# Kernel tuning notes

Hardware: AMD Instinct MI355X
Metric: run time of the kernel (lower is better)

The kernel has to match this reference:

```python
import jax, jax.numpy as jnp
import numpy as np

B, C, M, K, V, D, H, A, L, HF = 2, 128, 4, 4, 64, 1024, 16, 64, 4, 2048
E = M + K
EPS = 1e-5
THETA = 10000.0


def _rmsnorm(x, w):
    return x * jax.lax.rsqrt(jnp.mean(x * x, -1, keepdims=True) + EPS) * w


def _l2norm(x):
    n = jnp.sqrt(jnp.sum(x * x, -1, keepdims=True))
    return x / jnp.maximum(n, EPS)


def _rope(x, cos, sin):
    x1, x2 = jnp.split(x, 2, axis=-1)
    return jnp.concatenate([x1 * cos + x2 * sin, -x1 * sin + x2 * cos], -1)


def _forward(x_input, dec_w1, dec_w2, pos_emb, Wqkv, Wo, Wup, Wdown, attn_norm_w, ffn_norm_w, doc):
    b = x_input.shape[0]
    c = x_input.shape[1] // M
    # decoder_w1 then 'b (c m) (k v) -> b c k (m v)', decoder_w2, pos emb
    x = jnp.einsum('bsd,od->bso', x_input, dec_w1)
    x = x.reshape(b, c, M, K, V).transpose(0, 1, 3, 2, 4).reshape(b, c, K, M * V)
    x = jnp.einsum('bcku,du->bckd', x, dec_w2) + pos_emb
    # decoder_include_original_token: prepend original m tokens per block
    x = jnp.concatenate([x_input.reshape(b, c, M, D), x], axis=2).reshape(b, c * E, D)
    s = c * E
    # mask_mod (decoder_global_original_attn): (causal & kv%e<k & same_doc) | same_block
    idx = jnp.arange(s)
    blk = idx // E
    docs = doc[:, blk]  # [b, s]
    doc_m = docs[:, :, None] == docs[:, None, :]
    causal = blk[:, None] >= blk[None, :]
    kv_ok = (idx % E) < K
    same = blk[:, None] == blk[None, :]
    mask = (causal[None] & kv_ok[None, None, :] & doc_m) | same[None]  # [b, s, s]
    # rotary tables (applied post head-split, dim A)
    inv_freq = (1.0 / THETA) ** (jnp.arange(0, A, 2) / A)
    freqs = jnp.arange(s)[:, None] * inv_freq[None, :]
    cos, sin = jnp.cos(freqs), jnp.sin(freqs)  # [s, A/2]
    scale = 1.0 / jnp.sqrt(jnp.float32(A))
    neg = jnp.float32(-1e30)

    def heads(t):
        return t.reshape(b, s, H, A).transpose(0, 2, 1, 3)

    for li in range(L):
        xn = _rmsnorm(x, attn_norm_w[li])
        qkv = jnp.einsum('bsd,od->bso', xn, Wqkv[li])
        q, k, v = jnp.split(qkv, 3, axis=-1)
        q, k, v = heads(q), heads(k), heads(v)
        q, k = _l2norm(q), _l2norm(k)  # qk_norm
        q, k = _rope(q, cos, sin), _rope(k, cos, sin)
        scores = jnp.einsum('bhqa,bhka->bhqk', q, k) * scale
        scores = jnp.where(mask[:, None], scores, neg)
        probs = jax.nn.softmax(scores, axis=-1)
        attn = jnp.einsum('bhqk,bhka->bhqa', probs, v)
        attn = attn.transpose(0, 2, 1, 3).reshape(b, s, D)
        x1_in = jnp.einsum('bsd,od->bso', attn, Wo[li]) + x
        xf = _rmsnorm(x1_in, ffn_norm_w[li])
        up = jnp.einsum('bsd,od->bso', xf, Wup[li])
        u1, u2 = jnp.split(up, 2, axis=-1)
        x = jnp.einsum('bsh,dh->bsd', jax.nn.silu(u1) * u2, Wdown[li]) + x1_in
    # 'b (c e) d -> (b c) e d' then drop original tokens
    return x.reshape(b * c, E, D)[:, M:]


def setup_inputs() -> dict:
    key = jax.random.key(0)
    ks = jax.random.split(key, 10)
    sc = 0.02
    return {
        'x_input': jax.random.normal(ks[0], (B, C * M, D), jnp.float32),
        'doc': jnp.sort(jax.random.randint(ks[1], (B, C), 0, 4), axis=-1),
        'dec_w1': jax.random.normal(ks[2], (K * V, D), jnp.float32) * sc,
        'dec_w2': jax.random.normal(ks[3], (D, M * V), jnp.float32) * sc,
        'pos_emb': jax.random.normal(ks[4], (1, 1, K, D), jnp.float32) * sc,
        'Wqkv': jax.random.normal(ks[5], (L, 3 * D, D), jnp.float32) * sc,
        'Wo': jax.random.normal(ks[6], (L, D, D), jnp.float32) * sc,
        'Wup': jax.random.normal(ks[7], (L, 2 * HF, D), jnp.float32) * sc,
        'Wdown': jax.random.normal(ks[8], (L, D, HF), jnp.float32) * sc,
        'attn_norm_w': jnp.ones((L, D), jnp.float32),
        'ffn_norm_w': jnp.ones((L, D), jnp.float32),
    }


def reference(x_input, doc, dec_w1, dec_w2, pos_emb, Wqkv, Wo, Wup, Wdown, attn_norm_w, ffn_norm_w):
    return _forward(x_input, dec_w1, dec_w2, pos_emb, Wqkv, Wo, Wup, Wdown, attn_norm_w, ffn_norm_w, doc)
```

## Files before the change

kernel.cpp:

```cpp
#include <hip/hip_runtime.h>
#include <hip/hip_bf16.h>

typedef __bf16 bf16;
typedef __bf16 bf16x8 __attribute__((ext_vector_type(8)));
typedef __bf16 bf16x4 __attribute__((ext_vector_type(4)));
typedef float  f32x4  __attribute__((ext_vector_type(4)));

#define MFMA16(a, b, c) __builtin_amdgcn_mfma_f32_16x16x32_bf16(a, b, c, 0, 0, 0)

template <int EPI, int AF32, int BF32, int TM, int TN>
__global__ __launch_bounds__(256) void gemm_bt(
    const void* __restrict__ Av, const void* __restrict__ Bv,
    const float* __restrict__ Res, void* __restrict__ Out,
    int Ntot, int Ktot, int lda)
{
    constexpr int PA = TM / 64, PB = TN / 64;
    constexpr int WN = (TN == 128) ? ((TM == 128) ? 2 : 4) : 2;
    constexpr int WM = 4 / WN;
    constexpr int I = TM / (WM * 16), J = TN / (WN * 16);
    __shared__ __align__(16) bf16 As[2][TM][40];
    __shared__ __align__(16) bf16 Bs[2][TN][40];
    const int tid  = threadIdx.x;
    const int wave = tid >> 6, lane = tid & 63;
    const int quad = lane >> 4, l16 = lane & 15;
    const int wm = wave / WN, wn = wave % WN;
    const int rowW = wm * (TM / WM), colW = wn * (TN / WN);
    const int rowBase = blockIdx.y * TM, colBase = blockIdx.x * TN;

    f32x4 acc[I][J];
    const f32x4 z4 = {0.f, 0.f, 0.f, 0.f};
#pragma unroll
    for (int i = 0; i < I; i++)
#pragma unroll
        for (int j = 0; j < J; j++) acc[i][j] = z4;

    float4 rAf[PA][2]; bf16x8 rAb[PA];
    float4 rBf[PB][2]; bf16x8 rBb[PB];

    auto loadTile = [&](int kt) {
#pragma unroll
        for (int p = 0; p < PA; p++) {
            int ch = p * 256 + tid, r = ch >> 2, c8 = (ch & 3) << 3;
            if (AF32) {
                const float* s = (const float*)Av + (size_t)(rowBase + r) * lda + kt + c8;
                rAf[p][0] = *(const float4*)s; rAf[p][1] = *(const float4*)(s + 4);
            } else {
                rAb[p] = *(const bf16x8*)((const bf16*)Av + (size_t)(rowBase + r) * lda + kt + c8);
            }
        }
#pragma unroll
        for (int p = 0; p < PB; p++) {
            int ch = p * 256 + tid, r = ch >> 2, c8 = (ch & 3) << 3;
            if (BF32) {
                const float* s = (const float*)Bv + (size_t)(colBase + r) * Ktot + kt + c8;
                rBf[p][0] = *(const float4*)s; rBf[p][1] = *(const float4*)(s + 4);
            } else {
                rBb[p] = *(const bf16x8*)((const bf16*)Bv + (size_t)(colBase + r) * Ktot + kt + c8);
            }
        }
    };
    auto storeTile = [&](int buf) {
#pragma unroll
        for (int p = 0; p < PA; p++) {
            int ch = p * 256 + tid, r = ch >> 2, c8 = (ch & 3) << 3;
            bf16x8 t;
            if (AF32) {
                t[0]=(bf16)rAf[p][0].x; t[1]=(bf16)rAf[p][0].y; t[2]=(bf16)rAf[p][0].z; t[3]=(bf16)rAf[p][0].w;
                t[4]=(bf16)rAf[p][1].x; t[5]=(bf16)rAf[p][1].y; t[6]=(bf16)rAf[p][1].z; t[7]=(bf16)rAf[p][1].w;
            } else t = rAb[p];
            *(bf16x8*)&As[buf][r][c8] = t;
        }
#pragma unroll
        for (int p = 0; p < PB; p++) {
            int ch = p * 256 + tid, r = ch >> 2, c8 = (ch & 3) << 3;
            bf16x8 t;
            if (BF32) {
                t[0]=(bf16)rBf[p][0].x; t[1]=(bf16)rBf[p][0].y; t[2]=(bf16)rBf[p][0].z; t[3]=(bf16)rBf[p][0].w;
                t[4]=(bf16)rBf[p][1].x; t[5]=(bf16)rBf[p][1].y; t[6]=(bf16)rBf[p][1].z; t[7]=(bf16)rBf[p][1].w;
            } else t = rBb[p];
            *(bf16x8*)&Bs[buf][r][c8] = t;
        }
    };

    loadTile(0);
    storeTile(0);
    __syncthreads();
    const int nk = Ktot >> 5;
    for (int k = 0; k < nk; k++) {
        const bool more = (k + 1) < nk;
        if (more) loadTile((k + 1) << 5);
        const int buf = k & 1;
        bf16x8 af[I], bfr[J];
#pragma unroll
        for (int i = 0; i < I; i++)
            af[i] = *(const bf16x8*)&As[buf][rowW + i * 16 + l16][quad * 8];
#pragma unroll
        for (int j = 0; j < J; j++)
            bfr[j] = *(const bf16x8*)&Bs[buf][colW + j * 16 + l16][quad * 8];
#pragma unroll
        for (int i = 0; i < I; i++)
#pragma unroll
            for (int j = 0; j < J; j++)
                acc[i][j] = MFMA16(af[i], bfr[j], acc[i][j]);
        if (more) { storeTile(buf ^ 1); __syncthreads(); }
    }

#pragma unroll
    for (int i = 0; i < I; i++) {
        int row0 = rowBase + rowW + i * 16 + quad * 4;
#pragma unroll
        for (int j = 0; j < J; j++) {
            int col = colBase + colW + j * 16 + l16;
#pragma unroll
            for (int r = 0; r < 4; r++) {
                size_t off = (size_t)(row0 + r) * Ntot + col;
                float v = acc[i][j][r];
                if (EPI == 0)      ((bf16*)Out)[off]  = (bf16)v;
                else if (EPI == 1) ((float*)Out)[off] = v + Res[off];
                else               ((float*)Out)[off] = v;
            }
        }
    }
}

__global__ __launch_bounds__(256) void gemm_up_swiglu(
    const bf16* __restrict__ A, const float* __restrict__ B,
    bf16* __restrict__ Out)
{
    __shared__ __align__(16) bf16 As[2][128][40];
    __shared__ __align__(16) bf16 Bs[2][128][40];
    const int tid  = threadIdx.x;
    const int wave = tid >> 6, lane = tid & 63;
    const int quad = lane >> 4, l16 = lane & 15;
    const int wm = wave >> 1, wn = wave & 1;
    const int rowBase = blockIdx.y * 128, cb = blockIdx.x;

    f32x4 acc[4][4];
    const f32x4 z4 = {0.f, 0.f, 0.f, 0.f};
#pragma unroll
    for (int i = 0; i < 4; i++)
#pragma unroll
        for (int j = 0; j < 4; j++) acc[i][j] = z4;

    bf16x8 rA[2]; float4 rB[2][2];
    auto loadTile = [&](int kt) {
#pragma unroll
        for (int p = 0; p < 2; p++) {
            int ch = p * 256 + tid, r = ch >> 2, c8 = (ch & 3) << 3;
            rA[p] = *(const bf16x8*)(A + (size_t)(rowBase + r) * 1024 + kt + c8);
            int brow = (r >> 6) * 2048 + cb * 64 + (r & 63);
            const float* s = B + (size_t)brow * 1024 + kt + c8;
            rB[p][0] = *(const float4*)s; rB[p][1] = *(const float4*)(s + 4);
        }
    };
    auto storeTile = [&](int buf) {
#pragma unroll
        for (int p = 0; p < 2; p++) {
            int ch = p * 256 + tid, r = ch >> 2, c8 = (ch & 3) << 3;
            *(bf16x8*)&As[buf][r][c8] = rA[p];
            bf16x8 t;
            t[0]=(bf16)rB[p][0].x; t[1]=(bf16)rB[p][0].y; t[2]=(bf16)rB[p][0].z; t[3]=(bf16)rB[p][0].w;
            t[4]=(bf16)rB[p][1].x; t[5]=(bf16)rB[p][1].y; t[6]=(bf16)rB[p][1].z; t[7]=(bf16)rB[p][1].w;
            *(bf16x8*)&Bs[buf][r][c8] = t;
        }
    };

    loadTile(0);
    storeTile(0);
    __syncthreads();
    for (int k = 0; k < 32; k++) {
        const bool more = k < 31;
        if (more) loadTile((k + 1) << 5);
        const int buf = k & 1;
        bf16x8 af[4], bfr[4];
#pragma unroll
        for (int i = 0; i < 4; i++)
            af[i] = *(const bf16x8*)&As[buf][wm * 64 + i * 16 + l16][quad * 8];
#pragma unroll
        for (int j = 0; j < 4; j++) {
            int brow = (j < 2) ? (wn * 32 + j * 16) : (64 + wn * 32 + (j - 2) * 16);
            bfr[j] = *(const bf16x8*)&Bs[buf][brow + l16][quad * 8];
        }
#pragma unroll
        for (int i = 0; i < 4; i++)
#pragma unroll
            for (int j = 0; j < 4; j++)
                acc[i][j] = MFMA16(af[i], bfr[j], acc[i][j]);
        if (more) { storeTile(buf ^ 1); __syncthreads(); }
    }

#pragma unroll
    for (int i = 0; i < 4; i++) {
        int row0 = rowBase + wm * 64 + i * 16 + quad * 4;
#pragma unroll
        for (int jj = 0; jj < 2; jj++) {
            int col = cb * 64 + wn * 32 + jj * 16 + l16;
#pragma unroll
            for (int r = 0; r < 4; r++) {
                float u1 = acc[i][jj][r], u2 = acc[i][jj + 2][r];
                float g = u1 / (1.f + __expf(-u1));
                Out[(size_t)(row0 + r) * 2048 + col] = (bf16)(g * u2);
            }
        }
    }
}

__global__ __launch_bounds__(256) void rmsnorm_k(
    const float* __restrict__ X, const float* __restrict__ W,
    bf16* __restrict__ Out)
{
    const int row = blockIdx.x, tid = threadIdx.x;
    const float4 xv = *(const float4*)(X + (size_t)row * 1024 + tid * 4);
    float ss = xv.x * xv.x + xv.y * xv.y + xv.z * xv.z + xv.w * xv.w;
#pragma unroll
    for (int m = 1; m < 64; m <<= 1) ss += __shfl_xor(ss, m);
    __shared__ float red[4];
    if ((tid & 63) == 0) red[tid >> 6] = ss;
    __syncthreads();
    float tot = red[0] + red[1] + red[2] + red[3];
    float sc = rsqrtf(tot * (1.0f / 1024.0f) + 1e-5f);
    const float4 wv = *(const float4*)(W + tid * 4);
    bf16x4 o;
    o[0] = (bf16)(xv.x * sc * wv.x);
    o[1] = (bf16)(xv.y * sc * wv.y);
    o[2] = (bf16)(xv.z * sc * wv.z);
    o[3] = (bf16)(xv.w * sc * wv.w);
    *(bf16x4*)(Out + (size_t)row * 1024 + tid * 4) = o;
}

__global__ __launch_bounds__(256) void ropetab_k(float* __restrict__ tab)
{
    int i = blockIdx.x * 256 + threadIdx.x;
    int s = i >> 5, j = i & 31;
    float f = (float)s * __expf(-(float)j * 0.2878231366242557f);
    tab[i * 2]     = cosf(f);
    tab[i * 2 + 1] = sinf(f);
}

__global__ __launch_bounds__(256) void qkprep_k(
    bf16* __restrict__ qkv, const float* __restrict__ tab)
{
    int wid  = blockIdx.x * 4 + (threadIdx.x >> 6);
    int lane = threadIdx.x & 63;
    int s = wid & 1023, h = (wid >> 10) & 15, b = (wid >> 14) & 1, op = wid >> 15;
    bf16* addr = qkv + ((size_t)(b * 1024 + s)) * 3072 + op * 1024 + h * 64 + lane;
    float v = (float)*addr;
    float ss = v * v;
#pragma unroll
    for (int m = 1; m < 64; m <<= 1) ss += __shfl_xor(ss, m);
    v /= fmaxf(sqrtf(ss), 1e-5f);
    float2 cssn = ((const float2*)tab)[(s << 5) + (lane & 31)];
    float partner = __shfl_xor(v, 32);
    float o = (lane < 32) ? (v * cssn.x + partner * cssn.y)
                          : (v * cssn.x - partner * cssn.y);
    if (op == 0) o *= 0.125f;
    *addr = (bf16)o;
}

__global__ __launch_bounds__(256) void vtrans_k(
    const bf16* __restrict__ qkv, bf16* __restrict__ Vt)
{
    __shared__ __align__(16) bf16 Ls[64][72];
    const int st = blockIdx.x, h = blockIdx.y, b = blockIdx.z;
    const int tid = threadIdx.x;
#pragma unroll
    for (int p = 0; p < 2; p++) {
        int s = p * 32 + (tid >> 3), a0 = (tid & 7) << 3;
        *(bf16x8*)&Ls[s][a0] = *(const bf16x8*)(
            qkv + ((size_t)(b * 1024 + st * 64 + s)) * 3072 + 2048 + h * 64 + a0);
    }
    __syncthreads();
#pragma unroll
    for (int p = 0; p < 2; p++) {
        int a = p * 32 + (tid >> 3), s0 = (tid & 7) << 3;
        bf16x8 v;
#pragma unroll
        for (int j = 0; j < 8; j++) v[j] = Ls[s0 + j][a];
        *(bf16x8*)(Vt + (((size_t)((b * 16 + h) * 64 + a)) << 10) + st * 64 + s0) = v;
    }
}

__global__ __launch_bounds__(256) void attn_k(
    const bf16* __restrict__ qkv, const bf16* __restrict__ Vt,
    const int* __restrict__ doc, bf16* __restrict__ attnb)
{
    const int p = blockIdx.x, h = blockIdx.y, b = blockIdx.z;
    const int tid = threadIdx.x, w = tid >> 6, lane = tid & 63;
    const int quad = lane >> 4, l16 = lane & 15;
    __shared__ __align__(16) bf16 PsT[4][64][20];
    __shared__ int docL[128];
    if (tid < 128) docL[tid] = doc[b * 128 + tid];
    __syncthreads();

    const int g = (w == 0) ? p : (w == 1) ? 31 - p : (w == 2) ? 32 + p : 63 - p;
    const bf16* qp = qkv + ((size_t)(b * 1024 + g * 16 + l16)) * 3072 + h * 64 + quad * 8;
    const bf16x8 qf0 = *(const bf16x8*)qp;
    const bf16x8 qf1 = *(const bf16x8*)(qp + 32);
    const bf16* Kbase = qkv + ((size_t)(b * 1024)) * 3072 + 1024 + h * 64;
    const bf16* Vbase = Vt + (((size_t)((b * 16 + h) * 64)) << 10);

    const f32x4 z4 = {0.f, 0.f, 0.f, 0.f};
    f32x4 O[4] = {z4, z4, z4, z4};
    float lp[4] = {0.f, 0.f, 0.f, 0.f};

    int bq[4], dq[4];
#pragma unroll
    for (int r = 0; r < 4; r++) {
        bq[r] = (g * 16 + quad * 4 + r) >> 3;
        dq[r] = docL[bq[r]];
    }

    bf16x8 kc[8], kn[8];
    auto loadK = [&](int kt, bf16x8* dst) {
        const bf16* kp = Kbase + (size_t)(kt * 64 + l16) * 3072 + quad * 8;
#pragma unroll
        for (int kg = 0; kg < 4; kg++) {
            dst[kg * 2]     = *(const bf16x8*)(kp + (size_t)kg * 16 * 3072);
            dst[kg * 2 + 1] = *(const bf16x8*)(kp + (size_t)kg * 16 * 3072 + 32);
        }
    };

    const int tiles = (g + 4) >> 2;
    loadK(0, kc);
    for (int kt = 0; kt < tiles; kt++) {
        const int k0 = kt * 64;
        f32x4 sf[4];
#pragma unroll
        for (int kg = 0; kg < 4; kg++) {
            sf[kg] = z4;
            sf[kg] = MFMA16(qf0, kc[kg * 2],     sf[kg]);
            sf[kg] = MFMA16(qf1, kc[kg * 2 + 1], sf[kg]);
        }
        bf16x8 vr[4][2];
#pragma unroll
        for (int t = 0; t < 4; t++)
#pragma unroll
            for (int c = 0; c < 2; c++)
                vr[t][c] = *(const bf16x8*)(
                    Vbase + ((size_t)(t * 16 + l16) << 10) + k0 + c * 32 + quad * 8);
        if (kt + 1 < tiles) loadK(kt + 1, kn);

        float pvv[4][4];
#pragma unroll
        for (int kg = 0; kg < 4; kg++) {
            int kgi = k0 + kg * 16 + l16;
            int bk  = kgi >> 3;
            int dkv = docL[bk];
            bool kbit = (kgi & 7) < 4;
#pragma unroll
            for (int r = 0; r < 4; r++) {
                bool ok = (bq[r] == bk) || ((bq[r] >= bk) && kbit && (dq[r] == dkv));
                float pp = ok ? __expf(sf[kg][r]) : 0.f;
                pvv[kg][r] = pp;
                lp[r] += pp;
            }
        }
#pragma unroll
        for (int kg = 0; kg < 4; kg++) {
            bf16x4 t4;
#pragma unroll
            for (int r = 0; r < 4; r++) t4[r] = (bf16)pvv[kg][r];
            *(bf16x4*)&PsT[w][kg * 16 + l16][quad * 4] = t4;
        }
        bf16x8 pa0, pa1;
#pragma unroll
        for (int j = 0; j < 8; j++) {
            pa0[j] = PsT[w][quad * 8 + j][l16];
            pa1[j] = PsT[w][32 + quad * 8 + j][l16];
        }
#pragma unroll
        for (int t = 0; t < 4; t++) {
            O[t] = MFMA16(pa0, vr[t][0], O[t]);
            O[t] = MFMA16(pa1, vr[t][1], O[t]);
        }
        if (kt + 1 < tiles) {
#pragma unroll
            for (int i = 0; i < 8; i++) kc[i] = kn[i];
        }
    }

#pragma unroll
    for (int r = 0; r < 4; r++) {
#pragma unroll
        for (int m = 1; m < 16; m <<= 1) lp[r] += __shfl_xor(lp[r], m);
    }

#pragma unroll
    for (int t = 0; t < 4; t++)
#pragma unroll
        for (int r = 0; r < 4; r++) {
            int qg = g * 16 + quad * 4 + r;
            float v = O[t][r] / fmaxf(lp[r], 1e-20f);
            attnb[((size_t)(b * 1024) + qg) * 1024 + h * 64 + t * 16 + l16] = (bf16)v;
        }
}

__global__ __launch_bounds__(256) void permute_k(
    const bf16* __restrict__ t1, bf16* __restrict__ t1p)
{
    int idx = blockIdx.x * 256 + threadIdx.x;
    int u = idx & 255, m = u >> 6, v = u & 63;
    int orow = idx >> 8;
    int k = orow & 3, bc = orow >> 2;
    int b = bc >> 7, c = bc & 127;
    t1p[idx] = t1[((size_t)(b * 512 + c * 4 + m)) * 256 + k * 64 + v];
}

__global__ __launch_bounds__(256) void buildx_k(
    const float* __restrict__ x_input, const float* __restrict__ t2,
    const float* __restrict__ pos_emb, float* __restrict__ xres)
{
    int idx = blockIdx.x * 256 + threadIdx.x;
    int d = idx & 1023, row = idx >> 10;
    int b = row >> 10, rr = row & 1023;
    int c = rr >> 3, e = rr & 7;
    float v;
    if (e < 4)
        v = x_input[((size_t)(b * 512 + c * 4 + e)) * 1024 + d];
    else
        v = t2[((size_t)(b * 512 + c * 4 + (e - 4))) * 1024 + d] +
            pos_emb[(e - 4) * 1024 + d];
    xres[idx] = v;
}

__global__ __launch_bounds__(256) void finalout_k(
    const float* __restrict__ xres, float* __restrict__ out)
{
    int idx = blockIdx.x * 256 + threadIdx.x;
    int d = idx & 1023, t = idx >> 10;
    int kk = t & 3, bc = t >> 2;
    int b = bc >> 7, c = bc & 127;
    out[idx] = xres[((size_t)(b * 1024 + c * 8 + 4 + kk)) * 1024 + d];
}

extern "C" void kernel_launch(void* const* d_in, const int* in_sizes, int n_in,
                              void* d_out, int out_size, void* d_ws, size_t ws_size,
                              hipStream_t stream)
{
    const float* x_input = (const float*)d_in[0];
    const int*   doc     = (const int*)d_in[1];
    const float* dec_w1  = (const float*)d_in[2];
    const float* dec_w2  = (const float*)d_in[3];
    const float* pos_emb = (const float*)d_in[4];
    const float* Wqkv    = (const float*)d_in[5];
    const float* Wo      = (const float*)d_in[6];
    const float* Wup     = (const float*)d_in[7];
    const float* Wdown   = (const float*)d_in[8];
    const float* anw     = (const float*)d_in[9];
    const float* fnw     = (const float*)d_in[10];
    float* out = (float*)d_out;

    char* w = (char*)d_ws;
    float* xres  = (float*)(w);
    bf16*  attnb = (bf16*)(w + (8u << 20));
    bf16*  t1    = (bf16*)(w + (8u << 20));
    bf16*  t1p   = (bf16*)(w + (8u << 20) + (512u << 10));
    bf16*  Vt    = (bf16*)(w + (12u << 20));
    bf16*  xn2   = (bf16*)(w + (12u << 20));
    bf16*  qkv   = (bf16*)(w + (16u << 20));
    float* t2    = (float*)(w + (16u << 20));
    float* x1res = (float*)(w + (16u << 20));
    bf16*  hg    = (bf16*)(w + (24u << 20));
    bf16*  xn1   = (bf16*)(w + (28u << 20));
    float* rtab  = out;

    ropetab_k<<<128, 256, 0, stream>>>(rtab);
    gemm_bt<0, 1, 1, 64, 64><<<dim3(4, 16), 256, 0, stream>>>(
        x_input, dec_w1, nullptr, t1, 256, 1024, 1024);
    permute_k<<<1024, 256, 0, stream>>>(t1, t1p);
    gemm_bt<2, 0, 1, 64, 64><<<dim3(16, 16), 256, 0, stream>>>(
        t1p, dec_w2, nullptr, t2, 1024, 256, 256);
    buildx_k<<<8192, 256, 0, stream>>>(x_input, t2, pos_emb, xres);

    for (int li = 0; li < 4; ++li) {
        rmsnorm_k<<<2048, 256, 0, stream>>>(xres, anw + li * 1024, xn1);
        gemm_bt<0, 0, 1, 128, 128><<<dim3(24, 16), 256, 0, stream>>>(
            xn1, Wqkv + (size_t)li * 3072 * 1024, nullptr, qkv, 3072, 1024, 1024);
        qkprep_k<<<16384, 256, 0, stream>>>(qkv, rtab);
        vtrans_k<<<dim3(16, 16, 2), 256, 0, stream>>>(qkv, Vt);
        attn_k<<<dim3(16, 16, 2), 256, 0, stream>>>(qkv, Vt, doc, attnb);
        gemm_bt<1, 0, 1, 64, 64><<<dim3(16, 32), 256, 0, stream>>>(
            attnb, Wo + (size_t)li * 1024 * 1024, xres, x1res, 1024, 1024, 1024);
        rmsnorm_k<<<2048, 256, 0, stream>>>(x1res, fnw + li * 1024, xn2);
        gemm_up_swiglu<<<dim3(32, 16), 256, 0, stream>>>(
            xn2, Wup + (size_t)li * 4096 * 1024, hg);
        gemm_bt<1, 0, 1, 64, 64><<<dim3(16, 32), 256, 0, stream>>>(
            hg, Wdown + (size_t)li * 1024 * 2048, x1res, xres, 1024, 2048, 2048);
    }

    finalout_k<<<4096, 256, 0, stream>>>(xres, out);
}
```

Measured before the change: 1.000 ms.

## Split K across two wave groups within a block for Wo and Wdown GEMMs

Adds an intra-block split-K template parameter to the GEMM. With SK=2 the block runs 512 threads, and each 256-thread group reduces half of the K range into its own shared-memory tiles. The partial accumulators are then combined through shared memory before the residual epilogue. This targets the Wo and Wdown projections, whose 512-block grids with 64x64 tiles underfill the GPU and have long K loops. In exchange it doubles shared memory per block, adds a reduction step with extra syncs, and may lower the number of resident blocks.

After: 891.6 us. -10.8%, faster.

```diff
diff --git a/kernel.cpp b/kernel.cpp
--- a/kernel.cpp
+++ b/kernel.cpp
@@ -8,8 +8,8 @@
 
 #define MFMA16(a, b, c) __builtin_amdgcn_mfma_f32_16x16x32_bf16(a, b, c, 0, 0, 0)
 
-template <int EPI, int AF32, int BF32, int TM, int TN>
-__global__ __launch_bounds__(256) void gemm_bt(
+template <int EPI, int AF32, int BF32, int TM, int TN, int SK = 1>
+__global__ __launch_bounds__(256 * SK) void gemm_bt(
     const void* __restrict__ Av, const void* __restrict__ Bv,
     const float* __restrict__ Res, void* __restrict__ Out,
     int Ntot, int Ktot, int lda)
@@ -18,10 +18,13 @@
     constexpr int WN = (TN == 128) ? ((TM == 128) ? 2 : 4) : 2;
     constexpr int WM = 4 / WN;
     constexpr int I = TM / (WM * 16), J = TN / (WN * 16);
-    __shared__ __align__(16) bf16 As[2][TM][40];
-    __shared__ __align__(16) bf16 Bs[2][TN][40];
+    __shared__ __align__(16) bf16 As[2][SK][TM][40];
+    __shared__ __align__(16) bf16 Bs[2][SK][TN][40];
+    static_assert(SK == 1 || sizeof(As) >= TM * TN * 4, "combine buffer fits in As");
     const int tid  = threadIdx.x;
-    const int wave = tid >> 6, lane = tid & 63;
+    const int grp  = (SK > 1) ? (tid >> 8) : 0;
+    const int t8   = tid & 255;
+    const int wave = t8 >> 6, lane = tid & 63;
     const int quad = lane >> 4, l16 = lane & 15;
     const int wm = wave / WN, wn = wave % WN;
     const int rowW = wm * (TM / WM), colW = wn * (TN / WN);
@@ -40,7 +43,7 @@
     auto loadTile = [&](int kt) {
 #pragma unroll
         for (int p = 0; p < PA; p++) {
-            int ch = p * 256 + tid, r = ch >> 2, c8 = (ch & 3) << 3;
+            int ch = p * 256 + t8, r = ch >> 2, c8 = (ch & 3) << 3;
             if (AF32) {
                 const float* s = (const float*)Av + (size_t)(rowBase + r) * lda + kt + c8;
                 rAf[p][0] = *(const float4*)s; rAf[p][1] = *(const float4*)(s + 4);
@@ -50,7 +53,7 @@
         }
 #pragma unroll
         for (int p = 0; p < PB; p++) {
-            int ch = p * 256 + tid, r = ch >> 2, c8 = (ch & 3) << 3;
+            int ch = p * 256 + t8, r = ch >> 2, c8 = (ch & 3) << 3;
             if (BF32) {
                 const float* s = (const float*)Bv + (size_t)(colBase + r) * Ktot + kt + c8;
                 rBf[p][0] = *(const float4*)s; rBf[p][1] = *(const float4*)(s + 4);
@@ -62,47 +65,74 @@
     auto storeTile = [&](int buf) {
 #pragma unroll
         for (int p = 0; p < PA; p++) {
-            int ch = p * 256 + tid, r = ch >> 2, c8 = (ch & 3) << 3;
+            int ch = p * 256 + t8, r = ch >> 2, c8 = (ch & 3) << 3;
             bf16x8 t;
             if (AF32) {
                 t[0]=(bf16)rAf[p][0].x; t[1]=(bf16)rAf[p][0].y; t[2]=(bf16)rAf[p][0].z; t[3]=(bf16)rAf[p][0].w;
                 t[4]=(bf16)rAf[p][1].x; t[5]=(bf16)rAf[p][1].y; t[6]=(bf16)rAf[p][1].z; t[7]=(bf16)rAf[p][1].w;
             } else t = rAb[p];
-            *(bf16x8*)&As[buf][r][c8] = t;
+            *(bf16x8*)&As[buf][grp][r][c8] = t;
         }
 #pragma unroll
         for (int p = 0; p < PB; p++) {
-            int ch = p * 256 + tid, r = ch >> 2, c8 = (ch & 3) << 3;
+            int ch = p * 256 + t8, r = ch >> 2, c8 = (ch & 3) << 3;
             bf16x8 t;
             if (BF32) {
                 t[0]=(bf16)rBf[p][0].x; t[1]=(bf16)rBf[p][0].y; t[2]=(bf16)rBf[p][0].z; t[3]=(bf16)rBf[p][0].w;
                 t[4]=(bf16)rBf[p][1].x; t[5]=(bf16)rBf[p][1].y; t[6]=(bf16)rBf[p][1].z; t[7]=(bf16)rBf[p][1].w;
             } else t = rBb[p];
-            *(bf16x8*)&Bs[buf][r][c8] = t;
+            *(bf16x8*)&Bs[buf][grp][r][c8] = t;
         }
     };
 
-    loadTile(0);
+    const int Kgrp  = Ktot / SK;
+    const int kbase = grp * Kgrp;
+    loadTile(kbase);
     storeTile(0);
     __syncthreads();
-    const int nk = Ktot >> 5;
+    const int nk = Kgrp >> 5;
     for (int k = 0; k < nk; k++) {
         const bool more = (k + 1) < nk;
-        if (more) loadTile((k + 1) << 5);
+        if (more) loadTile(kbase + ((k + 1) << 5));
         const int buf = k & 1;
         bf16x8 af[I], bfr[J];
 #pragma unroll
         for (int i = 0; i < I; i++)
-            af[i] = *(const bf16x8*)&As[buf][rowW + i * 16 + l16][quad * 8];
+            af[i] = *(const bf16x8*)&As[buf][grp][rowW + i * 16 + l16][quad * 8];
 #pragma unroll
         for (int j = 0; j < J; j++)
-            bfr[j] = *(const bf16x8*)&Bs[buf][colW + j * 16 + l16][quad * 8];
+            bfr[j] = *(const bf16x8*)&Bs[buf][grp][colW + j * 16 + l16][quad * 8];
 #pragma unroll
         for (int i = 0; i < I; i++)
 #pragma unroll
             for (int j = 0; j < J; j++)
                 acc[i][j] = MFMA16(af[i], bfr[j], acc[i][j]);
         if (more) { storeTile(buf ^ 1); __syncthreads(); }
+    }
+
+    if (SK == 2) {
+        __syncthreads();
+        float* red = (float*)&As[0][0][0][0];
+        if (grp == 1) {
+#pragma unroll
+            for (int i = 0; i < I; i++)
+#pragma unroll
+                for (int j = 0; j < J; j++)
+#pragma unroll
+                    for (int r = 0; r < 4; r++)
+                        red[(rowW + i * 16 + quad * 4 + r) * TN +
+                            (colW + j * 16 + l16)] = acc[i][j][r];
+        }
+        __syncthreads();
+        if (grp != 0) return;
+#pragma unroll
+        for (int i = 0; i < I; i++)
+#pragma unroll
+            for (int j = 0; j < J; j++)
+#pragma unroll
+                for (int r = 0; r < 4; r++)
+                    acc[i][j][r] += red[(rowW + i * 16 + quad * 4 + r) * TN +
+                                        (colW + j * 16 + l16)];
     }
 
 #pragma unroll
@@ -479,12 +509,12 @@
         qkprep_k<<<16384, 256, 0, stream>>>(qkv, rtab);
         vtrans_k<<<dim3(16, 16, 2), 256, 0, stream>>>(qkv, Vt);
         attn_k<<<dim3(16, 16, 2), 256, 0, stream>>>(qkv, Vt, doc, attnb);
-        gemm_bt<1, 0, 1, 64, 64><<<dim3(16, 32), 256, 0, stream>>>(
+        gemm_bt<1, 0, 1, 64, 64, 2><<<dim3(16, 32), 512, 0, stream>>>(
             attnb, Wo + (size_t)li * 1024 * 1024, xres, x1res, 1024, 1024, 1024);
         rmsnorm_k<<<2048, 256, 0, stream>>>(x1res, fnw + li * 1024, xn2);
         gemm_up_swiglu<<<dim3(32, 16), 256, 0, stream>>>(
             xn2, Wup + (size_t)li * 4096 * 1024, hg);
-        gemm_bt<1, 0, 1, 64, 64><<<dim3(16, 32), 256, 0, stream>>>(
+        gemm_bt<1, 0, 1, 64, 64, 2><<<dim3(16, 32), 512, 0, stream>>>(
             hg, Wdown + (size_t)li * 1024 * 2048, x1res, xres, 1024, 2048, 2048);
     }
 
```
